# Optimization experiments

Hardware: AMD Instinct MI355X
Metric: run time of the kernel (lower is better)

Reference implementation:

```python
import jax, jax.numpy as jnp
import numpy as np

B, H, L, D = 4, 16, 8192, 64


def setup_inputs() -> dict:
    key = jax.random.key(0)
    ks = jax.random.split(key, 10)
    q = jax.random.normal(ks[0], (B, H, L, D), dtype=jnp.float32)
    k = jax.random.normal(ks[1], (B, H, L, D), dtype=jnp.float32)
    v = jax.random.normal(ks[2], (B, H, L, D), dtype=jnp.float32)
    mask = jax.random.randint(ks[3], (B, H, L), 0, 2, dtype=jnp.int32)
    s = 1.0 / np.sqrt(D)
    Wa_w = jax.random.uniform(ks[4], (D, D), jnp.float32, -s, s)  # torch Linear weight [out,in]
    Wa_b = jax.random.uniform(ks[5], (D,), jnp.float32, -s, s)
    Ua_w = jax.random.uniform(ks[6], (D, D), jnp.float32, -s, s)
    Ua_b = jax.random.uniform(ks[7], (D,), jnp.float32, -s, s)
    va_w = jax.random.uniform(ks[8], (1, D), jnp.float32, -s, s)
    va_b = jax.random.uniform(ks[9], (1,), jnp.float32, -s, s)
    return {"q": q, "k": k, "v": v, "mask": mask,
            "Wa_w": Wa_w, "Wa_b": Wa_b, "Ua_w": Ua_w, "Ua_b": Ua_b,
            "va_w": va_w, "va_b": va_b}


def reference(q, k, v, mask, Wa_w, Wa_b, Ua_w, Ua_b, va_w, va_b):
    # e1 = Wa(q), e2 = Ua(k)  (torch Linear: x @ W.T + b)
    e1 = jnp.einsum('bhld,ed->bhle', q, Wa_w) + Wa_b
    e2 = jnp.einsum('bhld,ed->bhle', k, Ua_w) + Ua_b
    t = jnp.tanh(e1 + e2)
    # va: [B,H,L,D] -> [B,H,L]
    e = jnp.einsum('bhld,d->bhl', t, va_w[0]) + va_b[0]
    e = jnp.where(mask == 0, jnp.float32(-10000.0), e)
    alpha = jax.nn.softmax(e, axis=-1)  # softmax over sequence length
    return alpha[..., None] * v
```

## Files before the change

### kernel.cpp

```cpp
#include <hip/hip_runtime.h>
#include <hip/hip_bf16.h>

#define BH   64
#define LSEQ 8192
#define DDIM 64
#define NPOS (BH * LSEQ)
#define NT4  (NPOS * DDIM / 4)

typedef __attribute__((ext_vector_type(8))) short bf16x8;
typedef __attribute__((ext_vector_type(4))) float f32x4;

__device__ inline short f2bf(float f) {
    __bf16 b = (__bf16)f;
    return __builtin_bit_cast(short, b);
}
__device__ inline float bf2f(short s) {
    unsigned u = ((unsigned)(unsigned short)s) << 16;
    return __builtin_bit_cast(float, u);
}
__device__ inline void split8(const float* f, bf16x8& hi, bf16x8& lo) {
#pragma unroll
    for (int j = 0; j < 8; j++) {
        short h = f2bf(f[j]);
        hi[j] = h;
        lo[j] = f2bf(f[j] - bf2f(h));
    }
}
__device__ inline float tanh_fast(float x) {
    float ex = __expf(2.f * x);
    return 1.f - 2.f * __builtin_amdgcn_rcpf(ex + 1.f);
}

__global__ __launch_bounds__(64, 2) void score_kernel(
    const float* __restrict__ q, const float* __restrict__ k,
    const int*   __restrict__ mask,
    const float* __restrict__ Waw, const float* __restrict__ Wab,
    const float* __restrict__ Uaw, const float* __restrict__ Uab,
    const float* __restrict__ vaw, const float* __restrict__ vab_p,
    float* __restrict__ e_out)
{
    const int lane = threadIdx.x;
    const int m    = lane & 15;
    const int g    = lane >> 4;
    const long t0  = (long)blockIdx.x * 4;

    __shared__ float lds[2][2048];

    bf16x8 bwa[4][2], bua[4][2];
    float bias_s[4], vav[4];
    float vab;

    float4 RA[8], RB[8];
    int4 mk0, mk1, mk2, mk3;

    auto gload = [&](float4 (&R)[8], int4& mk, long tile) {
        mk = ((const int4*)mask)[tile * 4 + g];
        const float* qb = q + tile * 1024;
        const float* kb = k + tile * 1024;
#pragma unroll
        for (int i = 0; i < 4; i++)
            R[i]     = *((const float4*)(qb + i * 256 + lane * 4));
#pragma unroll
        for (int i = 0; i < 4; i++)
            R[4 + i] = *((const float4*)(kb + i * 256 + lane * 4));
    };

    auto stage = [&](const float4 (&R)[8], int buf) {
#pragma unroll
        for (int i = 0; i < 8; i++) {
            const int row  = 4 * (i & 3) + g;
            const int half = i >> 2;
            float* dst = &lds[buf][half * 1024 + row * 64 + ((m ^ (row & 7)) << 2)];
            *((float4*)dst) = R[i];
        }
    };

    auto load_weights = [&]() {
#pragma unroll
        for (int t = 0; t < 4; t++) {
            const int n = t * 16 + m;
            bias_s[t] = Wab[n] + Uab[n];
            vav[t]    = vaw[n];
#pragma unroll
            for (int s = 0; s < 2; s++) {
                const int k0 = s * 32 + g * 8;
                const float4 wA = ((const float4*)(Waw + n * 64 + k0))[0];
                const float4 wB = ((const float4*)(Waw + n * 64 + k0))[1];
                const float4 uA = ((const float4*)(Uaw + n * 64 + k0))[0];
                const float4 uB = ((const float4*)(Uaw + n * 64 + k0))[1];
                float wf[8] = {wA.x, wA.y, wA.z, wA.w, wB.x, wB.y, wB.z, wB.w};
                float uf[8] = {uA.x, uA.y, uA.z, uA.w, uB.x, uB.y, uB.z, uB.w};
                bf16x8 wv, uv;
#pragma unroll
                for (int j = 0; j < 8; j++) { wv[j] = f2bf(wf[j]); uv[j] = f2bf(uf[j]); }
                bwa[t][s] = wv;
                bua[t][s] = uv;
            }
        }
        vab = vab_p[0];
    };

    auto compute = [&](int buf, const int4& mk, long tile) {
        f32x4 acc[4];
#pragma unroll
        for (int t = 0; t < 4; t++) acc[t] = (f32x4){0.f, 0.f, 0.f, 0.f};
        const float* L = lds[buf];
#pragma unroll
        for (int s = 0; s < 2; s++) {
            const int c0 = s * 8 + g * 2;
            const float4 qa = *((const float4*)(L + m * 64 + (( c0      ^ (m & 7)) << 2)));
            const float4 qb = *((const float4*)(L + m * 64 + (((c0 + 1) ^ (m & 7)) << 2)));
            const float4 ka = *((const float4*)(L + 1024 + m * 64 + (( c0      ^ (m & 7)) << 2)));
            const float4 kb = *((const float4*)(L + 1024 + m * 64 + (((c0 + 1) ^ (m & 7)) << 2)));
            float qf[8] = {qa.x, qa.y, qa.z, qa.w, qb.x, qb.y, qb.z, qb.w};
            float kf[8] = {ka.x, ka.y, ka.z, ka.w, kb.x, kb.y, kb.z, kb.w};
            bf16x8 qhi, qlo, khi, klo;
            split8(qf, qhi, qlo);
            split8(kf, khi, klo);
#pragma unroll
            for (int t = 0; t < 4; t++) {
                acc[t] = __builtin_amdgcn_mfma_f32_16x16x32_bf16(qhi, bwa[t][s], acc[t], 0, 0, 0);
                acc[t] = __builtin_amdgcn_mfma_f32_16x16x32_bf16(qlo, bwa[t][s], acc[t], 0, 0, 0);
                acc[t] = __builtin_amdgcn_mfma_f32_16x16x32_bf16(khi, bua[t][s], acc[t], 0, 0, 0);
                acc[t] = __builtin_amdgcn_mfma_f32_16x16x32_bf16(klo, bua[t][s], acc[t], 0, 0, 0);
            }
        }
        float c[4] = {0.f, 0.f, 0.f, 0.f};
#pragma unroll
        for (int t = 0; t < 4; t++) {
#pragma unroll
            for (int r = 0; r < 4; r++)
                c[r] += vav[t] * tanh_fast(acc[t][r] + bias_s[t]);
        }
#pragma unroll
        for (int r = 0; r < 4; r++) {
#pragma unroll
            for (int off2 = 1; off2 < 16; off2 <<= 1)
                c[r] += __shfl_xor(c[r], off2, 16);
        }
        if (m == 0) {
            float4 ev;
            ev.x = mk.x ? c[0] + vab : -10000.f;
            ev.y = mk.y ? c[1] + vab : -10000.f;
            ev.z = mk.z ? c[2] + vab : -10000.f;
            ev.w = mk.w ? c[3] + vab : -10000.f;
            *((float4*)(e_out + tile * 16 + g * 4)) = ev;
        }
    };

    gload(RA, mk0, t0 + 0);
    gload(RB, mk1, t0 + 1);
    load_weights();
    stage(RA, 0);
    gload(RA, mk2, t0 + 2);
    stage(RB, 1);
    gload(RB, mk3, t0 + 3);
    compute(0, mk0, t0 + 0);
    stage(RA, 0);
    compute(1, mk1, t0 + 1);
    stage(RB, 1);
    compute(0, mk2, t0 + 2);
    compute(1, mk3, t0 + 3);
}

__global__ __launch_bounds__(1024) void rowstat_kernel(
    const float* __restrict__ e, float* __restrict__ stats)
{
    const int row = blockIdx.x;
    const size_t base = (size_t)row * LSEQ;
    const int tid  = threadIdx.x;
    const int lane = tid & 63;
    const int wv   = tid >> 6;
    __shared__ float redmax[16];
    __shared__ float redsum[16];

    float4 e0 = ((const float4*)(e + base))[tid];
    float4 e1 = ((const float4*)(e + base))[1024 + tid];
    float em[8] = {e0.x, e0.y, e0.z, e0.w, e1.x, e1.y, e1.z, e1.w};

    float lm = em[0];
#pragma unroll
    for (int j = 1; j < 8; j++) lm = fmaxf(lm, em[j]);
#pragma unroll
    for (int off = 32; off >= 1; off >>= 1) lm = fmaxf(lm, __shfl_xor(lm, off, 64));
    if (lane == 0) redmax[wv] = lm;
    __syncthreads();
    float M = redmax[0];
#pragma unroll
    for (int i = 1; i < 16; i++) M = fmaxf(M, redmax[i]);

    float ls = 0.f;
#pragma unroll
    for (int j = 0; j < 8; j++) ls += __expf(em[j] - M);
#pragma unroll
    for (int off = 32; off >= 1; off >>= 1) ls += __shfl_xor(ls, off, 64);
    if (lane == 0) redsum[wv] = ls;
    __syncthreads();
    if (tid == 0) {
        float S = 0.f;
#pragma unroll
        for (int i = 0; i < 16; i++) S += redsum[i];
        stats[row * 2]     = M;
        stats[row * 2 + 1] = 1.f / S;
    }
}

__global__ __launch_bounds__(256) void scale_kernel(
    const float* __restrict__ v, const float* __restrict__ e,
    const float* __restrict__ stats, float* __restrict__ out)
{
    const size_t b0 = (size_t)blockIdx.x * 1024 + threadIdx.x;
    const f32x4* vp = (const f32x4*)v;
    f32x4*       op = (f32x4*)out;

    size_t idx[4];
    f32x4  vv[4];
    float  ee[4];
    float2 st[4];
#pragma unroll
    for (int j = 0; j < 4; j++) {
        idx[j] = b0 + (size_t)j * 256;
        vv[j]  = __builtin_nontemporal_load(vp + idx[j]);
    }
#pragma unroll
    for (int j = 0; j < 4; j++) {
        const size_t p = idx[j] >> 4;
        ee[j] = e[p];
        st[j] = ((const float2*)stats)[p >> 13];
    }
#pragma unroll
    for (int j = 0; j < 4; j++) {
        const float a = __expf(ee[j] - st[j].x) * st[j].y;
        f32x4 o = vv[j] * a;
        __builtin_nontemporal_store(o, op + idx[j]);
    }
}

extern "C" void kernel_launch(void* const* d_in, const int* in_sizes, int n_in,
                              void* d_out, int out_size, void* d_ws, size_t ws_size,
                              hipStream_t stream) {
    const float* q    = (const float*)d_in[0];
    const float* k    = (const float*)d_in[1];
    const float* v    = (const float*)d_in[2];
    const int*   mask = (const int*)d_in[3];
    const float* Waw  = (const float*)d_in[4];
    const float* Wab  = (const float*)d_in[5];
    const float* Uaw  = (const float*)d_in[6];
    const float* Uab  = (const float*)d_in[7];
    const float* vaw  = (const float*)d_in[8];
    const float* vab  = (const float*)d_in[9];
    float* out = (float*)d_out;

    float* e_buf = (float*)d_ws;
    float* stats = (float*)d_ws + NPOS;

    score_kernel<<<NPOS / 64, 64, 0, stream>>>(q, k, mask, Waw, Wab, Uaw, Uab, vaw, vab, e_buf);
    rowstat_kernel<<<BH, 1024, 0, stream>>>(e_buf, stats);
    scale_kernel<<<NT4 / 1024, 256, 0, stream>>>(v, e_buf, stats, out);
}
```

Measured before the change: 472.4 us.

## Load q/k tiles directly into LDS via global_load_lds with manual vmcnt waits

Result: faster. 414.3 us (-12.3%).

```diff
diff --git a/kernel.cpp b/kernel.cpp
--- a/kernel.cpp
+++ b/kernel.cpp
@@ -48,56 +48,49 @@
 
     bf16x8 bwa[4][2], bua[4][2];
     float bias_s[4], vav[4];
-    float vab;
-
-    float4 RA[8], RB[8];
-    int4 mk0, mk1, mk2, mk3;
-
-    auto gload = [&](float4 (&R)[8], int4& mk, long tile) {
-        mk = ((const int4*)mask)[tile * 4 + g];
+#pragma unroll
+    for (int t = 0; t < 4; t++) {
+        const int n = t * 16 + m;
+        bias_s[t] = Wab[n] + Uab[n];
+        vav[t]    = vaw[n];
+#pragma unroll
+        for (int s = 0; s < 2; s++) {
+            const int k0 = s * 32 + g * 8;
+            const float4 wA = ((const float4*)(Waw + n * 64 + k0))[0];
+            const float4 wB = ((const float4*)(Waw + n * 64 + k0))[1];
+            const float4 uA = ((const float4*)(Uaw + n * 64 + k0))[0];
+            const float4 uB = ((const float4*)(Uaw + n * 64 + k0))[1];
+            float wf[8] = {wA.x, wA.y, wA.z, wA.w, wB.x, wB.y, wB.z, wB.w};
+            float uf[8] = {uA.x, uA.y, uA.z, uA.w, uB.x, uB.y, uB.z, uB.w};
+            bf16x8 wv, uv;
+#pragma unroll
+            for (int j = 0; j < 8; j++) { wv[j] = f2bf(wf[j]); uv[j] = f2bf(uf[j]); }
+            bwa[t][s] = wv;
+            bua[t][s] = uv;
+        }
+    }
+    const float vab = vab_p[0];
+    const int4 mk0 = ((const int4*)mask)[(t0 + 0) * 4 + g];
+    const int4 mk1 = ((const int4*)mask)[(t0 + 1) * 4 + g];
+    const int4 mk2 = ((const int4*)mask)[(t0 + 2) * 4 + g];
+    const int4 mk3 = ((const int4*)mask)[(t0 + 3) * 4 + g];
+
+    auto issue_tile = [&](long tile, int buf) {
         const float* qb = q + tile * 1024;
         const float* kb = k + tile * 1024;
 #pragma unroll
-        for (int i = 0; i < 4; i++)
-            R[i]     = *((const float4*)(qb + i * 256 + lane * 4));
-#pragma unroll
-        for (int i = 0; i < 4; i++)
-            R[4 + i] = *((const float4*)(kb + i * 256 + lane * 4));
-    };
-
-    auto stage = [&](const float4 (&R)[8], int buf) {
-#pragma unroll
-        for (int i = 0; i < 8; i++) {
-            const int row  = 4 * (i & 3) + g;
-            const int half = i >> 2;
-            float* dst = &lds[buf][half * 1024 + row * 64 + ((m ^ (row & 7)) << 2)];
-            *((float4*)dst) = R[i];
-        }
-    };
-
-    auto load_weights = [&]() {
-#pragma unroll
-        for (int t = 0; t < 4; t++) {
-            const int n = t * 16 + m;
-            bias_s[t] = Wab[n] + Uab[n];
-            vav[t]    = vaw[n];
-#pragma unroll
-            for (int s = 0; s < 2; s++) {
-                const int k0 = s * 32 + g * 8;
-                const float4 wA = ((const float4*)(Waw + n * 64 + k0))[0];
-                const float4 wB = ((const float4*)(Waw + n * 64 + k0))[1];
-                const float4 uA = ((const float4*)(Uaw + n * 64 + k0))[0];
-                const float4 uB = ((const float4*)(Uaw + n * 64 + k0))[1];
-                float wf[8] = {wA.x, wA.y, wA.z, wA.w, wB.x, wB.y, wB.z, wB.w};
-                float uf[8] = {uA.x, uA.y, uA.z, uA.w, uB.x, uB.y, uB.z, uB.w};
-                bf16x8 wv, uv;
-#pragma unroll
-                for (int j = 0; j < 8; j++) { wv[j] = f2bf(wf[j]); uv[j] = f2bf(uf[j]); }
-                bwa[t][s] = wv;
-                bua[t][s] = uv;
-            }
-        }
-        vab = vab_p[0];
+        for (int i = 0; i < 4; i++) {
+            const int row = 4 * i + g;
+            const int c   = m ^ (row & 7);
+            __builtin_amdgcn_global_load_lds(
+                (const __attribute__((address_space(1))) void*)(qb + row * 64 + c * 4),
+                (__attribute__((address_space(3))) void*)(&lds[buf][i * 256]),
+                16, 0, 0);
+            __builtin_amdgcn_global_load_lds(
+                (const __attribute__((address_space(1))) void*)(kb + row * 64 + c * 4),
+                (__attribute__((address_space(3))) void*)(&lds[buf][1024 + i * 256]),
+                16, 0, 0);
+        }
     };
 
     auto compute = [&](int buf, const int4& mk, long tile) {
@@ -148,18 +141,21 @@
         }
     };
 
-    gload(RA, mk0, t0 + 0);
-    gload(RB, mk1, t0 + 1);
-    load_weights();
-    stage(RA, 0);
-    gload(RA, mk2, t0 + 2);
-    stage(RB, 1);
-    gload(RB, mk3, t0 + 3);
+    issue_tile(t0 + 0, 0);
+    issue_tile(t0 + 1, 1);
+    asm volatile("s_waitcnt vmcnt(8)" ::: "memory");
+    __builtin_amdgcn_sched_barrier(0);
     compute(0, mk0, t0 + 0);
-    stage(RA, 0);
+    issue_tile(t0 + 2, 0);
+    asm volatile("s_waitcnt vmcnt(9)" ::: "memory");
+    __builtin_amdgcn_sched_barrier(0);
     compute(1, mk1, t0 + 1);
-    stage(RB, 1);
+    issue_tile(t0 + 3, 1);
+    asm volatile("s_waitcnt vmcnt(9)" ::: "memory");
+    __builtin_amdgcn_sched_barrier(0);
     compute(0, mk2, t0 + 2);
+    asm volatile("s_waitcnt vmcnt(1)" ::: "memory");
+    __builtin_amdgcn_sched_barrier(0);
     compute(1, mk3, t0 + 3);
 }
 
```
